# Kernel tuning notes

Measured on AMD Instinct MI355X. Metric: run time of the kernel, lower is better.

Reference implementation:

```python
import jax, jax.numpy as jnp
import numpy as np

N, E, D, DE, H = 50000, 400000, 128, 64, 8
EPS = 1e-5
SLOPE = 0.2


def setup_inputs() -> dict:
    key = jax.random.key(0)
    ks = jax.random.split(key, 16)

    def lin(k, fan_in, fan_out):
        return (jax.random.normal(k, (fan_in, fan_out), jnp.float32) / np.sqrt(fan_in)).astype(jnp.float32)

    return {
        "node_features": jax.random.normal(ks[0], (N, D), jnp.float32),
        "edge_features": jax.random.normal(ks[1], (E, DE), jnp.float32),
        "Wn": lin(ks[2], D, D), "bn": jnp.zeros((D,), jnp.float32),
        "Wq": lin(ks[3], D, D), "bq": jnp.zeros((D,), jnp.float32),
        "Wk": lin(ks[4], D, D), "bk": jnp.zeros((D,), jnp.float32),
        "Wv": lin(ks[5], D, D), "bv": jnp.zeros((D,), jnp.float32),
        "We": lin(ks[6], DE, D), "be": jnp.zeros((D,), jnp.float32),
        "A1": lin(ks[7], 3 * D, D), "b1": jnp.zeros((D,), jnp.float32),
        "A2": lin(ks[8], D, H), "b2": jnp.zeros((H,), jnp.float32),
        "gamma": jnp.ones((D,), jnp.float32),
        "beta": jnp.zeros((D,), jnp.float32),
        "edge_index": jax.random.randint(ks[9], (2, E), 0, N, dtype=jnp.int32),
    }


def reference(node_features, edge_features, Wn, bn, Wq, bq, Wk, bk, Wv, bv,
              We, be, A1, b1, A2, b2, gamma, beta, edge_index):
    num_nodes = node_features.shape[0]
    h = node_features @ Wn + bn                      # [N, D]
    q = node_features @ Wq + bq                      # [N, D]
    k = node_features @ Wk + bk                      # [N, D]
    v = node_features @ Wv + bv                      # [N, D]
    eh = edge_features @ We + be                     # [E, D]

    src, tgt = edge_index[0], edge_index[1]
    attn_in = jnp.concatenate([q[src], k[tgt], eh], axis=-1)   # [E, 3D]
    hmid = jax.nn.leaky_relu(attn_in @ A1 + b1, SLOPE)          # [E, D]
    scores = jax.nn.leaky_relu(hmid @ A2 + b2, SLOPE)           # [E, H]
    w = jax.nn.softmax(scores.mean(axis=-1), axis=0)            # global softmax over edges, [E]

    # scatter-add: output[src] += w * v[tgt]
    out = jax.ops.segment_sum(w[:, None] * v[tgt], src, num_segments=num_nodes)  # [N, D]

    y = h + out                                       # dropout = identity (eval)
    mu = y.mean(axis=-1, keepdims=True)
    var = y.var(axis=-1, keepdims=True)
    return gamma * (y - mu) / jnp.sqrt(var + EPS) + beta
```

## Files before the change

### kernel.cpp

```cpp
#include <hip/hip_runtime.h>

#define D 128
#define DE 64
#define SLOPE 0.2f
#define EPS 1e-5f

typedef float f32x4 __attribute__((ext_vector_type(4)));
typedef short bf16x8 __attribute__((ext_vector_type(8)));
typedef unsigned short ushort;

__device__ __forceinline__ float lrelu(float x) { return x > 0.f ? x : SLOPE * x; }

__device__ __forceinline__ ushort f2bf(float x) {
  union { float f; unsigned u; } c; c.f = x;
  unsigned r = c.u + 0x7FFFu + ((c.u >> 16) & 1u);
  return (ushort)(r >> 16);
}
__device__ __forceinline__ float bf2f(unsigned u) {
  return __uint_as_float(u << 16);
}
__device__ __forceinline__ uint4 cvt8(const float* p) {
  float4 f0 = *(const float4*)p;
  float4 f1 = *(const float4*)(p + 4);
  union { ushort us[8]; uint4 v; } u;
  u.us[0] = f2bf(f0.x); u.us[1] = f2bf(f0.y);
  u.us[2] = f2bf(f0.z); u.us[3] = f2bf(f0.w);
  u.us[4] = f2bf(f1.x); u.us[5] = f2bf(f1.y);
  u.us[6] = f2bf(f1.z); u.us[7] = f2bf(f1.w);
  return u.v;
}

__global__ __launch_bounds__(128) void fold_pack(
    const float* __restrict__ Wq, const float* __restrict__ Wk,
    const float* __restrict__ We, const float* __restrict__ A1,
    const float* __restrict__ bq, const float* __restrict__ bk,
    const float* __restrict__ be, const float* __restrict__ b1,
    const float* __restrict__ Wn, const float* __restrict__ Wv,
    ushort* __restrict__ AfqT, ushort* __restrict__ AfkT,
    ushort* __restrict__ AfeT, float* __restrict__ bfold,
    ushort* __restrict__ WnT, ushort* __restrict__ WvT,
    const int* __restrict__ src, int* __restrict__ deg, int E) {
  int r = blockIdx.x;
  int j = threadIdx.x;
  if (r < 128) {
    float acc = 0.f;
    for (int t = 0; t < 128; ++t) acc += Wq[r * 128 + t] * A1[t * 128 + j];
    AfqT[j * 128 + r] = f2bf(acc);
  } else if (r < 256) {
    int k = r - 128;
    float acc = 0.f;
    for (int t = 0; t < 128; ++t) acc += Wk[k * 128 + t] * A1[(128 + t) * 128 + j];
    AfkT[j * 128 + k] = f2bf(acc);
  } else if (r < 320) {
    int k = r - 256;
    float acc = 0.f;
    for (int t = 0; t < 128; ++t) acc += We[k * 128 + t] * A1[(256 + t) * 128 + j];
    AfeT[j * 64 + k] = f2bf(acc);
  } else if (r == 320) {
    float acc = b1[j];
    for (int t = 0; t < 128; ++t) {
      acc += bq[t] * A1[t * 128 + j];
      acc += bk[t] * A1[(128 + t) * 128 + j];
      acc += be[t] * A1[(256 + t) * 128 + j];
    }
    bfold[j] = acc;
  } else if (r < 449) {
    int c = r - 321;
    WnT[c * 128 + j] = f2bf(Wn[j * 128 + c]);
  } else if (r < 577) {
    int c = r - 449;
    WvT[c * 128 + j] = f2bf(Wv[j * 128 + c]);
  } else {
    int i = (r - 577) * 128 + j;
    if (i < E) atomicAdd(&deg[src[i]], 1);
  }
}

__global__ __launch_bounds__(256, 2) void node_gemm_mfma(
    const float* __restrict__ X, const ushort* __restrict__ WnT,
    const ushort* __restrict__ WvT, const ushort* __restrict__ AfqT,
    const ushort* __restrict__ AfkT, const float* __restrict__ bn,
    const float* __restrict__ bv, float* __restrict__ h,
    ushort* __restrict__ vb, ushort* __restrict__ q2p,
    ushort* __restrict__ k2p, int Nn) {
  __shared__ ushort As[256 * 40];
  __shared__ ushort Bs[128 * 40];
  __shared__ float bS[128];
  const ushort* WT;
  const float* bb = nullptr;
  float* O = nullptr;
  ushort* Ob = nullptr;
  int mode;
  switch (blockIdx.y) {
    case 0: WT = WnT; bb = bn; O = h; mode = 0; break;
    case 1: WT = WvT; bb = bv; Ob = vb; mode = 1; break;
    case 2: WT = AfqT; Ob = q2p; mode = 2; break;
    default: WT = AfkT; Ob = k2p; mode = 2; break;
  }
  const int t = threadIdx.x;
  if (t < 128) bS[t] = bb ? bb[t] : 0.f;
  const int seg = t & 3, arow = t >> 2;
  const int m0 = blockIdx.x * 256;
  int rIdx[4];
#pragma unroll
  for (int l = 0; l < 4; ++l) rIdx[l] = min(m0 + arow + 64 * l, Nn - 1);
  uint4 avA[4], avB[2];
#pragma unroll
  for (int l = 0; l < 4; ++l)
    avA[l] = cvt8(X + (size_t)rIdx[l] * 128 + seg * 8);
#pragma unroll
  for (int l = 0; l < 2; ++l)
    avB[l] = *(const uint4*)(WT + (arow + 64 * l) * 128 + seg * 8);
  f32x4 acc[4][8];
#pragma unroll
  for (int mt = 0; mt < 4; ++mt)
#pragma unroll
    for (int nt = 0; nt < 8; ++nt) acc[mt][nt] = (f32x4)(0.f);
  const int lane = t & 63, wv = t >> 6, l15 = lane & 15, quad = lane >> 4;
  for (int ch = 0; ch < 4; ++ch) {
#pragma unroll
    for (int l = 0; l < 4; ++l)
      *(uint4*)&As[(arow + 64 * l) * 40 + seg * 8] = avA[l];
#pragma unroll
    for (int l = 0; l < 2; ++l)
      *(uint4*)&Bs[(arow + 64 * l) * 40 + seg * 8] = avB[l];
    __syncthreads();
    if (ch < 3) {
      int o = (ch + 1) * 32 + seg * 8;
#pragma unroll
      for (int l = 0; l < 4; ++l)
        avA[l] = cvt8(X + (size_t)rIdx[l] * 128 + o);
#pragma unroll
      for (int l = 0; l < 2; ++l)
        avB[l] = *(const uint4*)(WT + (arow + 64 * l) * 128 + o);
    }
    bf16x8 af[4];
#pragma unroll
    for (int mt = 0; mt < 4; ++mt)
      af[mt] = *(const bf16x8*)&As[(wv * 64 + mt * 16 + l15) * 40 + quad * 8];
#pragma unroll
    for (int nt = 0; nt < 8; ++nt) {
      bf16x8 bfr = *(const bf16x8*)&Bs[(nt * 16 + l15) * 40 + quad * 8];
#pragma unroll
      for (int mt = 0; mt < 4; ++mt)
        acc[mt][nt] =
            __builtin_amdgcn_mfma_f32_16x16x32_bf16(af[mt], bfr, acc[mt][nt], 0, 0, 0);
    }
    __syncthreads();
  }
#pragma unroll
  for (int mt = 0; mt < 4; ++mt) {
    int rowb = m0 + wv * 64 + mt * 16 + quad * 4;
#pragma unroll
    for (int nt = 0; nt < 8; ++nt) {
      int col = nt * 16 + l15;
      float b = bS[col];
#pragma unroll
      for (int r = 0; r < 4; ++r) {
        int rg = rowb + r;
        if (rg < Nn) {
          if (mode == 0)      O[(size_t)rg * 128 + col] = acc[mt][nt][r] + b;
          else if (mode == 1) Ob[(size_t)rg * 128 + col] = f2bf(acc[mt][nt][r] + b);
          else                Ob[(size_t)rg * 128 + l15 * 8 + nt] = f2bf(acc[mt][nt][r]);
        }
      }
    }
  }
}

__global__ __launch_bounds__(256, 3) void edge_fused4(
    const float* __restrict__ EF, const ushort* __restrict__ AfeT,
    const float* __restrict__ bfold, const float* __restrict__ A2,
    const float* __restrict__ b2, const ushort* __restrict__ q2p,
    const ushort* __restrict__ k2p, const int* __restrict__ src,
    const int* __restrict__ tgt, int* __restrict__ cursor,
    int2* __restrict__ cwt, float2* __restrict__ part, int E) {
  __shared__ ushort As[128 * 40];
  __shared__ ushort Bs[128 * 40];
  __shared__ float A2s[128 * 9];
  __shared__ float bfS[128];
  __shared__ float b2s[8];
  __shared__ int sIdxS[128], sIdxT[128];
  __shared__ float redM[16], redS[16];
  const int t = threadIdx.x;
  const int e0 = blockIdx.x * 128;
  if (t < 128) {
    sIdxS[t] = src[min(e0 + t, E - 1)];
    bfS[t] = bfold[t];
  } else {
    sIdxT[t - 128] = tgt[min(e0 + t - 128, E - 1)];
  }
  if (t < 8) b2s[t] = b2[t];
#pragma unroll
  for (int l = 0; l < 4; ++l) {
    int i = t + l * 256;
    A2s[(i >> 3) * 9 + (i & 7)] = A2[i];
  }
  const int seg = t & 3, arow = t >> 2;
  int ecl[2];
#pragma unroll
  for (int l = 0; l < 2; ++l) ecl[l] = min(e0 + arow + 64 * l, E - 1);
  uint4 avA[2], avB[2];
#pragma unroll
  for (int l = 0; l < 2; ++l) {
    avA[l] = cvt8(EF + (size_t)ecl[l] * 64 + seg * 8);
    avB[l] = *(const uint4*)(AfeT + (arow + 64 * l) * 64 + seg * 8);
  }
  f32x4 acc[2][8];
#pragma unroll
  for (int mt = 0; mt < 2; ++mt)
#pragma unroll
    for (int nt = 0; nt < 8; ++nt) acc[mt][nt] = (f32x4)(0.f);
  const int lane = t & 63, wv = t >> 6, l15 = lane & 15, quad = lane >> 4;

#pragma unroll
  for (int ch = 0; ch < 2; ++ch) {
#pragma unroll
    for (int l = 0; l < 2; ++l) {
      *(uint4*)&As[(arow + 64 * l) * 40 + seg * 8] = avA[l];
      *(uint4*)&Bs[(arow + 64 * l) * 40 + seg * 8] = avB[l];
    }
    __syncthreads();
    if (ch == 0) {
      int o = 32 + seg * 8;
#pragma unroll
      for (int l = 0; l < 2; ++l) {
        avA[l] = cvt8(EF + (size_t)ecl[l] * 64 + o);
        avB[l] = *(const uint4*)(AfeT + (arow + 64 * l) * 64 + o);
      }
    }
    bf16x8 af[2];
#pragma unroll
    for (int mt = 0; mt < 2; ++mt)
      af[mt] = *(const bf16x8*)&As[(wv * 32 + mt * 16 + l15) * 40 + quad * 8];
#pragma unroll
    for (int nt = 0; nt < 8; ++nt) {
      bf16x8 bfr = *(const bf16x8*)&Bs[(nt * 16 + l15) * 40 + quad * 8];
#pragma unroll
      for (int mt = 0; mt < 2; ++mt)
        acc[mt][nt] =
            __builtin_amdgcn_mfma_f32_16x16x32_bf16(af[mt], bfr, acc[mt][nt], 0, 0, 0);
    }
    if (ch == 0) __syncthreads();
  }

  float bfv[8];
#pragma unroll
  for (int nt = 0; nt < 8; ++nt) bfv[nt] = bfS[nt * 16 + l15];
#pragma unroll
  for (int mt = 0; mt < 2; ++mt) {
#pragma unroll
    for (int r = 0; r < 4; ++r) {
      int erow = wv * 32 + mt * 16 + quad * 4 + r;
      int si = sIdxS[erow], ti = sIdxT[erow];
      uint4 qv = *(const uint4*)(q2p + (size_t)si * 128 + l15 * 8);
      uint4 kv = *(const uint4*)(k2p + (size_t)ti * 128 + l15 * 8);
      const ushort* qs = (const ushort*)&qv;
      const ushort* ks = (const ushort*)&kv;
#pragma unroll
      for (int nt = 0; nt < 8; ++nt)
        acc[mt][nt][r] =
            lrelu(acc[mt][nt][r] + bf2f(qs[nt]) + bf2f(ks[nt]) + bfv[nt]);
    }
  }
  float tacc[2][4];
#pragma unroll
  for (int mt = 0; mt < 2; ++mt)
#pragma unroll
    for (int r = 0; r < 4; ++r) tacc[mt][r] = 0.f;
  for (int hh = 0; hh < 8; ++hh) {
    float a2v[8];
#pragma unroll
    for (int nt = 0; nt < 8; ++nt) a2v[nt] = A2s[nt * 144 + l15 * 9 + hh];
    float b2h = b2s[hh];
#pragma unroll
    for (int mt = 0; mt < 2; ++mt)
#pragma unroll
      for (int r = 0; r < 4; ++r) {
        float p = 0.f;
#pragma unroll
        for (int nt = 0; nt < 8; ++nt) p += acc[mt][nt][r] * a2v[nt];
        p += __shfl_xor(p, 1);
        p += __shfl_xor(p, 2);
        p += __shfl_xor(p, 4);
        p += __shfl_xor(p, 8);
        tacc[mt][r] += lrelu(p + b2h);
      }
  }
  if (l15 == 0) {
    float sc[8];
    float m = -1e30f;
#pragma unroll
    for (int mt = 0; mt < 2; ++mt)
#pragma unroll
      for (int r = 0; r < 4; ++r) {
        int i = mt * 4 + r;
        sc[i] = tacc[mt][r] * 0.125f;
        int e = e0 + wv * 32 + mt * 16 + quad * 4 + r;
        if (e < E) m = fmaxf(m, sc[i]);
      }
    float ssum = 0.f;
#pragma unroll
    for (int mt = 0; mt < 2; ++mt)
#pragma unroll
      for (int r = 0; r < 4; ++r) {
        int i = mt * 4 + r;
        int erow = wv * 32 + mt * 16 + quad * 4 + r;
        if (e0 + erow < E) {
          ssum += __expf(sc[i] - m);
          int j = atomicAdd(&cursor[sIdxS[erow]], 1);
          cwt[j] = make_int2(sIdxT[erow], __float_as_int(sc[i]));
        }
      }
    int rid = wv * 4 + quad;
    redM[rid] = m;
    redS[rid] = ssum;
  }
  __syncthreads();
  if (t == 0) {
    float M = redM[0], S = redS[0];
#pragma unroll
    for (int i = 1; i < 16; ++i) {
      float m2 = redM[i], s2 = redS[i];
      float Mn = fmaxf(M, m2);
      S = S * __expf(M - Mn) + s2 * __expf(m2 - Mn);
      M = Mn;
    }
    part[blockIdx.x] = make_float2(M, S);
  }
}

__global__ __launch_bounds__(256) void softmax_final(
    const float2* __restrict__ part, int nPart, float* __restrict__ MS) {
  __shared__ float mS[256], sS[256];
  int tid = threadIdx.x;
  float m = -1e30f, sum = 0.f;
  for (int i = tid; i < nPart; i += 256) {
    float2 p = part[i];
    float M = fmaxf(m, p.x);
    sum = sum * __expf(m - M) + p.y * __expf(p.x - M);
    m = M;
  }
  mS[tid] = m;
  sS[tid] = sum;
  __syncthreads();
  for (int off = 128; off > 0; off >>= 1) {
    if (tid < off) {
      float m1 = mS[tid], s1 = sS[tid];
      float m2 = mS[tid + off], s2 = sS[tid + off];
      float M = fmaxf(m1, m2);
      mS[tid] = M;
      sS[tid] = s1 * __expf(m1 - M) + s2 * __expf(m2 - M);
    }
    __syncthreads();
  }
  if (tid == 0) {
    MS[0] = mS[0];
    MS[1] = 1.f / sS[0];
  }
}

__global__ __launch_bounds__(256) void scan1(const int* __restrict__ deg,
                                             int* __restrict__ incl,
                                             int* __restrict__ bsum, int N) {
  __shared__ int sh[256];
  int tid = threadIdx.x;
  int i = blockIdx.x * 256 + tid;
  sh[tid] = (i < N) ? deg[i] : 0;
  __syncthreads();
  for (int off = 1; off < 256; off <<= 1) {
    int tv = (tid >= off) ? sh[tid - off] : 0;
    __syncthreads();
    sh[tid] += tv;
    __syncthreads();
  }
  if (i < N) incl[i] = sh[tid];
  if (tid == 255) bsum[blockIdx.x] = sh[255];
}

__global__ __launch_bounds__(256) void scan2(int* __restrict__ bsum, int nb) {
  __shared__ int sh[256];
  int tid = threadIdx.x;
  sh[tid] = (tid < nb) ? bsum[tid] : 0;
  __syncthreads();
  for (int off = 1; off < 256; off <<= 1) {
    int tv = (tid >= off) ? sh[tid - off] : 0;
    __syncthreads();
    sh[tid] += tv;
    __syncthreads();
  }
  if (tid < nb) bsum[tid] = sh[tid];
}

__global__ __launch_bounds__(256) void scan3(const int* __restrict__ deg,
                                             const int* __restrict__ incl,
                                             const int* __restrict__ bsum,
                                             int* __restrict__ offs,
                                             int* __restrict__ cursor, int N,
                                             int E) {
  int i = blockIdx.x * 256 + threadIdx.x;
  if (i >= N) return;
  int base = (blockIdx.x > 0) ? bsum[blockIdx.x - 1] : 0;
  int ex = incl[i] - deg[i] + base;
  offs[i] = ex;
  cursor[i] = ex;
  if (i == N - 1) offs[N] = E;
}

__global__ __launch_bounds__(256) void gather_ln(
    const int* __restrict__ offs, const int2* __restrict__ cwt,
    const ushort* __restrict__ vb, const float* __restrict__ MS,
    const float* __restrict__ gamma, const float* __restrict__ beta,
    float* __restrict__ y, int N) {
  int tid = threadIdx.x;
  int n = blockIdx.x * 4 + (tid >> 6);
  if (n >= N) return;
  int lane = tid & 63;
  float M = MS[0], inv = MS[1];
  int beg = offs[n], end = offs[n + 1];
  float a0 = 0.f, a1 = 0.f;
  int j = beg;
  for (; j + 4 <= end; j += 4) {
    int2 p0 = cwt[j], p1 = cwt[j + 1], p2 = cwt[j + 2], p3 = cwt[j + 3];
    unsigned u0 = *(const unsigned*)(vb + (size_t)p0.x * 128 + lane * 2);
    unsigned u1 = *(const unsigned*)(vb + (size_t)p1.x * 128 + lane * 2);
    unsigned u2 = *(const unsigned*)(vb + (size_t)p2.x * 128 + lane * 2);
    unsigned u3 = *(const unsigned*)(vb + (size_t)p3.x * 128 + lane * 2);
    float w0 = __expf(__int_as_float(p0.y) - M) * inv;
    float w1 = __expf(__int_as_float(p1.y) - M) * inv;
    float w2 = __expf(__int_as_float(p2.y) - M) * inv;
    float w3 = __expf(__int_as_float(p3.y) - M) * inv;
    a0 += w0 * bf2f(u0 & 0xffffu) + w1 * bf2f(u1 & 0xffffu) +
          w2 * bf2f(u2 & 0xffffu) + w3 * bf2f(u3 & 0xffffu);
    a1 += w0 * bf2f(u0 >> 16) + w1 * bf2f(u1 >> 16) + w2 * bf2f(u2 >> 16) +
          w3 * bf2f(u3 >> 16);
  }
  for (; j < end; ++j) {
    int2 p = cwt[j];
    float w = __expf(__int_as_float(p.y) - M) * inv;
    unsigned u = *(const unsigned*)(vb + (size_t)p.x * 128 + lane * 2);
    a0 += w * bf2f(u & 0xffffu);
    a1 += w * bf2f(u >> 16);
  }
  size_t base = (size_t)n * 128 + lane * 2;
  float2 hv = *(const float2*)(y + base);
  float y0 = hv.x + a0, y1 = hv.y + a1;
  float sum = y0 + y1, ssq = y0 * y0 + y1 * y1;
#pragma unroll
  for (int off = 1; off < 64; off <<= 1) {
    sum += __shfl_xor(sum, off);
    ssq += __shfl_xor(ssq, off);
  }
  float mu = sum * (1.f / 128.f);
  float var = ssq * (1.f / 128.f) - mu * mu;
  float rstd = rsqrtf(var + EPS);
  float2 g = *(const float2*)(gamma + lane * 2);
  float2 bt = *(const float2*)(beta + lane * 2);
  float2 out;
  out.x = g.x * (y0 - mu) * rstd + bt.x;
  out.y = g.y * (y1 - mu) * rstd + bt.y;
  *(float2*)(y + base) = out;
}

extern "C" void kernel_launch(void* const* d_in, const int* in_sizes, int n_in,
                              void* d_out, int out_size, void* d_ws,
                              size_t ws_size, hipStream_t stream) {
  const float* X  = (const float*)d_in[0];
  const float* EF = (const float*)d_in[1];
  const float* Wn = (const float*)d_in[2];
  const float* bn = (const float*)d_in[3];
  const float* Wq = (const float*)d_in[4];
  const float* bq = (const float*)d_in[5];
  const float* Wk = (const float*)d_in[6];
  const float* bk = (const float*)d_in[7];
  const float* Wv = (const float*)d_in[8];
  const float* bv = (const float*)d_in[9];
  const float* We = (const float*)d_in[10];
  const float* be = (const float*)d_in[11];
  const float* A1 = (const float*)d_in[12];
  const float* b1 = (const float*)d_in[13];
  const float* A2 = (const float*)d_in[14];
  const float* b2 = (const float*)d_in[15];
  const float* gamma = (const float*)d_in[16];
  const float* beta  = (const float*)d_in[17];
  const int* ei = (const int*)d_in[18];

  int N = in_sizes[0] / D;
  int E = in_sizes[1] / DE;
  const int* src = ei;
  const int* tgt = ei + E;

  float* h = (float*)d_out;
  float* ws = (float*)d_ws;
  float2* part = (float2*)ws;
  float* MS    = (float*)(part + 4096);
  float* bfold = MS + 4;
  ushort* vb   = (ushort*)(bfold + 128);
  ushort* q2p  = vb + (size_t)N * D;
  ushort* k2p  = q2p + (size_t)N * D;
  ushort* AfqT = k2p + (size_t)N * D;
  ushort* AfkT = AfqT + 128 * 128;
  ushort* AfeT = AfkT + 128 * 128;
  ushort* WnT  = AfeT + 128 * 64;
  ushort* WvT  = WnT + 128 * 128;
  int* deg    = (int*)(WvT + 128 * 128);
  int* incl   = deg + N;
  int* bsum   = incl + N;
  int* cursor = bsum + 256;
  int* offs   = cursor + N;
  int2* cwt   = (int2*)(offs + N + 2);

  int nbScan = (N + 255) / 256;
  int nbEdge = (E + 127) / 128;
  int nbHist = (E + 127) / 128;

  hipMemsetAsync(deg, 0, (size_t)N * sizeof(int), stream);
  fold_pack<<<577 + nbHist, 128, 0, stream>>>(Wq, Wk, We, A1, bq, bk, be, b1,
                                              Wn, Wv, AfqT, AfkT, AfeT, bfold,
                                              WnT, WvT, src, deg, E);
  scan1<<<nbScan, 256, 0, stream>>>(deg, incl, bsum, N);
  scan2<<<1, 256, 0, stream>>>(bsum, nbScan);
  scan3<<<nbScan, 256, 0, stream>>>(deg, incl, bsum, offs, cursor, N, E);
  node_gemm_mfma<<<dim3((N + 255) / 256, 4), 256, 0, stream>>>(
      X, WnT, WvT, AfqT, AfkT, bn, bv, h, vb, q2p, k2p, N);
  edge_fused4<<<nbEdge, 256, 0, stream>>>(EF, AfeT, bfold, A2, b2, q2p, k2p,
                                          src, tgt, cursor, cwt, part, E);
  softmax_final<<<1, 256, 0, stream>>>(part, nbEdge, MS);
  gather_ln<<<(N + 3) / 4, 256, 0, stream>>>(offs, cwt, vb, MS, gamma, beta, h,
                                             N);
}
```

Measured before the change: 387.3 us.

## Prepack node GEMM weights in MFMA fragment order and halve row tile

The fold/pack kernel now writes Wn, Wv and the folded q/k weights in a layout that matches the per-lane MFMA B-fragment order, so the node GEMM reads B fragments straight from global memory (cache) instead of staging them through shared memory. The row tile per block drops from 256 to 128, halving the A staging buffer and accumulator registers and doubling the grid. This removes the B shared-memory stores and loads and raises parallelism, at the cost of repeated global/L2 reads of the weights per block.

New measurement: 381.1 us. No clear change (-1.6%).

```diff
diff --git a/kernel.cpp b/kernel.cpp
--- a/kernel.cpp
+++ b/kernel.cpp
@@ -36,21 +36,23 @@
     const float* __restrict__ bq, const float* __restrict__ bk,
     const float* __restrict__ be, const float* __restrict__ b1,
     const float* __restrict__ Wn, const float* __restrict__ Wv,
-    ushort* __restrict__ AfqT, ushort* __restrict__ AfkT,
+    ushort* __restrict__ AfqP, ushort* __restrict__ AfkP,
     ushort* __restrict__ AfeT, float* __restrict__ bfold,
-    ushort* __restrict__ WnT, ushort* __restrict__ WvT,
+    ushort* __restrict__ WnP, ushort* __restrict__ WvP,
     const int* __restrict__ src, int* __restrict__ deg, int E) {
   int r = blockIdx.x;
   int j = threadIdx.x;
   if (r < 128) {
     float acc = 0.f;
     for (int t = 0; t < 128; ++t) acc += Wq[r * 128 + t] * A1[t * 128 + j];
-    AfqT[j * 128 + r] = f2bf(acc);
+    int ch = r >> 5, quad = (r >> 3) & 3, jj = r & 7, nt = j >> 4, l15 = j & 15;
+    AfqP[(((ch * 8 + nt) * 4 + quad) * 16 + l15) * 8 + jj] = f2bf(acc);
   } else if (r < 256) {
     int k = r - 128;
     float acc = 0.f;
     for (int t = 0; t < 128; ++t) acc += Wk[k * 128 + t] * A1[(128 + t) * 128 + j];
-    AfkT[j * 128 + k] = f2bf(acc);
+    int ch = k >> 5, quad = (k >> 3) & 3, jj = k & 7, nt = j >> 4, l15 = j & 15;
+    AfkP[(((ch * 8 + nt) * 4 + quad) * 16 + l15) * 8 + jj] = f2bf(acc);
   } else if (r < 320) {
     int k = r - 256;
     float acc = 0.f;
@@ -66,10 +68,12 @@
     bfold[j] = acc;
   } else if (r < 449) {
     int c = r - 321;
-    WnT[c * 128 + j] = f2bf(Wn[j * 128 + c]);
+    int ch = j >> 5, quad = (j >> 3) & 3, jj = j & 7, nt = c >> 4, l15 = c & 15;
+    WnP[(((ch * 8 + nt) * 4 + quad) * 16 + l15) * 8 + jj] = f2bf(Wn[j * 128 + c]);
   } else if (r < 577) {
     int c = r - 449;
-    WvT[c * 128 + j] = f2bf(Wv[j * 128 + c]);
+    int ch = j >> 5, quad = (j >> 3) & 3, jj = j & 7, nt = c >> 4, l15 = c & 15;
+    WvP[(((ch * 8 + nt) * 4 + quad) * 16 + l15) * 8 + jj] = f2bf(Wv[j * 128 + c]);
   } else {
     int i = (r - 577) * 128 + j;
     if (i < E) atomicAdd(&deg[src[i]], 1);
@@ -77,80 +81,71 @@
 }
 
 __global__ __launch_bounds__(256, 2) void node_gemm_mfma(
-    const float* __restrict__ X, const ushort* __restrict__ WnT,
-    const ushort* __restrict__ WvT, const ushort* __restrict__ AfqT,
-    const ushort* __restrict__ AfkT, const float* __restrict__ bn,
+    const float* __restrict__ X, const ushort* __restrict__ WnP,
+    const ushort* __restrict__ WvP, const ushort* __restrict__ AfqP,
+    const ushort* __restrict__ AfkP, const float* __restrict__ bn,
     const float* __restrict__ bv, float* __restrict__ h,
     ushort* __restrict__ vb, ushort* __restrict__ q2p,
     ushort* __restrict__ k2p, int Nn) {
-  __shared__ ushort As[256 * 40];
-  __shared__ ushort Bs[128 * 40];
+  __shared__ ushort As[128 * 40];
   __shared__ float bS[128];
-  const ushort* WT;
+  const ushort* BP;
   const float* bb = nullptr;
   float* O = nullptr;
   ushort* Ob = nullptr;
   int mode;
   switch (blockIdx.y) {
-    case 0: WT = WnT; bb = bn; O = h; mode = 0; break;
-    case 1: WT = WvT; bb = bv; Ob = vb; mode = 1; break;
-    case 2: WT = AfqT; Ob = q2p; mode = 2; break;
-    default: WT = AfkT; Ob = k2p; mode = 2; break;
+    case 0: BP = WnP; bb = bn; O = h; mode = 0; break;
+    case 1: BP = WvP; bb = bv; Ob = vb; mode = 1; break;
+    case 2: BP = AfqP; Ob = q2p; mode = 2; break;
+    default: BP = AfkP; Ob = k2p; mode = 2; break;
   }
   const int t = threadIdx.x;
   if (t < 128) bS[t] = bb ? bb[t] : 0.f;
   const int seg = t & 3, arow = t >> 2;
-  const int m0 = blockIdx.x * 256;
-  int rIdx[4];
-#pragma unroll
-  for (int l = 0; l < 4; ++l) rIdx[l] = min(m0 + arow + 64 * l, Nn - 1);
-  uint4 avA[4], avB[2];
-#pragma unroll
-  for (int l = 0; l < 4; ++l)
+  const int m0 = blockIdx.x * 128;
+  int rIdx[2];
+#pragma unroll
+  for (int l = 0; l < 2; ++l) rIdx[l] = min(m0 + arow + 64 * l, Nn - 1);
+  uint4 avA[2];
+#pragma unroll
+  for (int l = 0; l < 2; ++l)
     avA[l] = cvt8(X + (size_t)rIdx[l] * 128 + seg * 8);
-#pragma unroll
-  for (int l = 0; l < 2; ++l)
-    avB[l] = *(const uint4*)(WT + (arow + 64 * l) * 128 + seg * 8);
-  f32x4 acc[4][8];
-#pragma unroll
-  for (int mt = 0; mt < 4; ++mt)
+  f32x4 acc[2][8];
+#pragma unroll
+  for (int mt = 0; mt < 2; ++mt)
 #pragma unroll
     for (int nt = 0; nt < 8; ++nt) acc[mt][nt] = (f32x4)(0.f);
   const int lane = t & 63, wv = t >> 6, l15 = lane & 15, quad = lane >> 4;
   for (int ch = 0; ch < 4; ++ch) {
 #pragma unroll
-    for (int l = 0; l < 4; ++l)
+    for (int l = 0; l < 2; ++l)
       *(uint4*)&As[(arow + 64 * l) * 40 + seg * 8] = avA[l];
-#pragma unroll
-    for (int l = 0; l < 2; ++l)
-      *(uint4*)&Bs[(arow + 64 * l) * 40 + seg * 8] = avB[l];
     __syncthreads();
     if (ch < 3) {
       int o = (ch + 1) * 32 + seg * 8;
 #pragma unroll
-      for (int l = 0; l < 4; ++l)
+      for (int l = 0; l < 2; ++l)
         avA[l] = cvt8(X + (size_t)rIdx[l] * 128 + o);
-#pragma unroll
-      for (int l = 0; l < 2; ++l)
-        avB[l] = *(const uint4*)(WT + (arow + 64 * l) * 128 + o);
-    }
-    bf16x8 af[4];
-#pragma unroll
-    for (int mt = 0; mt < 4; ++mt)
-      af[mt] = *(const bf16x8*)&As[(wv * 64 + mt * 16 + l15) * 40 + quad * 8];
+    }
+    bf16x8 af[2];
+#pragma unroll
+    for (int mt = 0; mt < 2; ++mt)
+      af[mt] = *(const bf16x8*)&As[(wv * 32 + mt * 16 + l15) * 40 + quad * 8];
+    const ushort* bp = BP + ((size_t)(ch * 8) * 64 + lane) * 8;
 #pragma unroll
     for (int nt = 0; nt < 8; ++nt) {
-      bf16x8 bfr = *(const bf16x8*)&Bs[(nt * 16 + l15) * 40 + quad * 8];
-#pragma unroll
-      for (int mt = 0; mt < 4; ++mt)
+      bf16x8 bfr = *(const bf16x8*)(bp + nt * 512);
+#pragma unroll
+      for (int mt = 0; mt < 2; ++mt)
         acc[mt][nt] =
             __builtin_amdgcn_mfma_f32_16x16x32_bf16(af[mt], bfr, acc[mt][nt], 0, 0, 0);
     }
     __syncthreads();
   }
 #pragma unroll
-  for (int mt = 0; mt < 4; ++mt) {
-    int rowb = m0 + wv * 64 + mt * 16 + quad * 4;
+  for (int mt = 0; mt < 2; ++mt) {
+    int rowb = m0 + wv * 32 + mt * 16 + quad * 4;
 #pragma unroll
     for (int nt = 0; nt < 8; ++nt) {
       int col = nt * 16 + l15;
@@ -498,12 +493,12 @@
   ushort* vb   = (ushort*)(bfold + 128);
   ushort* q2p  = vb + (size_t)N * D;
   ushort* k2p  = q2p + (size_t)N * D;
-  ushort* AfqT = k2p + (size_t)N * D;
-  ushort* AfkT = AfqT + 128 * 128;
-  ushort* AfeT = AfkT + 128 * 128;
-  ushort* WnT  = AfeT + 128 * 64;
-  ushort* WvT  = WnT + 128 * 128;
-  int* deg    = (int*)(WvT + 128 * 128);
+  ushort* AfqP = k2p + (size_t)N * D;
+  ushort* AfkP = AfqP + 128 * 128;
+  ushort* AfeT = AfkP + 128 * 128;
+  ushort* WnP  = AfeT + 128 * 64;
+  ushort* WvP  = WnP + 128 * 128;
+  int* deg    = (int*)(WvP + 128 * 128);
   int* incl   = deg + N;
   int* bsum   = incl + N;
   int* cursor = bsum + 256;
@@ -516,13 +511,13 @@
 
   hipMemsetAsync(deg, 0, (size_t)N * sizeof(int), stream);
   fold_pack<<<577 + nbHist, 128, 0, stream>>>(Wq, Wk, We, A1, bq, bk, be, b1,
-                                              Wn, Wv, AfqT, AfkT, AfeT, bfold,
-                                              WnT, WvT, src, deg, E);
+                                              Wn, Wv, AfqP, AfkP, AfeT, bfold,
+                                              WnP, WvP, src, deg, E);
   scan1<<<nbScan, 256, 0, stream>>>(deg, incl, bsum, N);
   scan2<<<1, 256, 0, stream>>>(bsum, nbScan);
   scan3<<<nbScan, 256, 0, stream>>>(deg, incl, bsum, offs, cursor, N, E);
-  node_gemm_mfma<<<dim3((N + 255) / 256, 4), 256, 0, stream>>>(
-      X, WnT, WvT, AfqT, AfkT, bn, bv, h, vb, q2p, k2p, N);
+  node_gemm_mfma<<<dim3((N + 127) / 128, 4), 256, 0, stream>>>(
+      X, WnP, WvP, AfqP, AfkP, bn, bv, h, vb, q2p, k2p, N);
   edge_fused4<<<nbEdge, 256, 0, stream>>>(EF, AfeT, bfold, A2, b2, q2p, k2p,
                                           src, tgt, cursor, cwt, part, E);
   softmax_final<<<1, 256, 0, stream>>>(part, nbEdge, MS);
```
